# Kernel tuning notes

Measured on AMD Instinct MI355X. Metric: run time of the kernel, lower is better.

The kernel has to match this reference:

```python
import jax, jax.numpy as jnp
import numpy as np

H = 4  # num_heads in every nn.MultiheadAttention


def _mha_self(x, mask, w_in, b_in, w_out, b_out):
    # x: [N, L, E], mask: [N, L] (1 = valid). Matches torch nn.MultiheadAttention
    # self-attention with key_padding_mask, dropout=0 (eval).
    N, L, E = x.shape
    d = E // H
    qkv = x @ w_in.T + b_in                      # [N, L, 3E]
    q, k, v = jnp.split(qkv, 3, axis=-1)
    q = q.reshape(N, L, H, d)
    k = k.reshape(N, L, H, d)
    v = v.reshape(N, L, H, d)
    scale = 1.0 / float(np.sqrt(d))
    scores = jnp.einsum('nlhd,nmhd->nhlm', q, k) * scale
    scores = jnp.where(mask[:, None, None, :] > 0, scores, jnp.float32(-1e9))
    a = jax.nn.softmax(scores, axis=-1)
    o = jnp.einsum('nhlm,nmhd->nlhd', a, v).reshape(N, L, E)
    return o @ w_out.T + b_out


def _mha_cross_seq(q_x, kv_x, w_in, b_in, w_out, b_out):
    # torch MHA called with [B,1,E] tensors (batch_first=False): sequence length = B.
    E = q_x.shape[-1]
    d = E // H
    wq, wk, wv = jnp.split(w_in, 3, axis=0)
    bq, bk, bv = jnp.split(b_in, 3, axis=0)
    q = (q_x @ wq.T + bq).reshape(-1, H, d)
    k = (kv_x @ wk.T + bk).reshape(-1, H, d)
    v = (kv_x @ wv.T + bv).reshape(-1, H, d)
    scale = 1.0 / float(np.sqrt(d))
    a = jax.nn.softmax(jnp.einsum('lhd,mhd->hlm', q, k) * scale, axis=-1)
    o = jnp.einsum('hlm,mhd->lhd', a, v).reshape(-1, E)
    return o @ w_out.T + b_out


def _masked_mean(x, m):
    # (attn_out * mask).sum / (mask.sum + 1e-10); yields 0 for fully-masked rows,
    # matching the torch zero-embedding branches.
    return (x * m[..., None]).sum(axis=1) / (m.sum(axis=1, keepdims=True) + 1e-10)


def _ln(x, g, b, eps=1e-5):
    mu = x.mean(-1, keepdims=True)
    var = ((x - mu) ** 2).mean(-1, keepdims=True)
    return (x - mu) / jnp.sqrt(var + eps) * g + b


def setup_inputs():
    key = jax.random.key(0)
    ks = iter(jax.random.split(key, 48))
    B, S, T, W, E = 8, 8, 16, 64, 768
    F, FD = 20, 256

    def rnd(shape, scale):
        return jax.random.normal(next(ks), shape, jnp.float32) * scale

    inp = {}
    inp['word_embeddings'] = rnd((B, S, T, W, E), 1.0)
    inp['attention_mask'] = jax.random.randint(next(ks), (B, S, T, W), 0, 2, jnp.int32)
    inp['handcrafted_features'] = rnd((B, F), 1.0)
    for name in ('word', 'sent', 'sec'):
        inp[name + '_w_in'] = rnd((3 * E, E), 1.0 / np.sqrt(E))
        inp[name + '_b_in'] = jnp.zeros((3 * E,), jnp.float32)
        inp[name + '_w_out'] = rnd((E, E), 1.0 / np.sqrt(E))
        inp[name + '_b_out'] = jnp.zeros((E,), jnp.float32)
    inp['bp_w'] = rnd((FD, E), 1.0 / np.sqrt(E)); inp['bp_b'] = jnp.zeros((FD,), jnp.float32)
    inp['hp_w'] = rnd((FD, F), 1.0 / np.sqrt(F)); inp['hp_b'] = jnp.zeros((FD,), jnp.float32)
    inp['fa_w_in'] = rnd((3 * FD, FD), 1.0 / np.sqrt(FD)); inp['fa_b_in'] = jnp.zeros((3 * FD,), jnp.float32)
    inp['fa_w_out'] = rnd((FD, FD), 1.0 / np.sqrt(FD)); inp['fa_b_out'] = jnp.zeros((FD,), jnp.float32)
    inp['gate_w'] = rnd((FD, 2 * FD), 1.0 / np.sqrt(2 * FD)); inp['gate_b'] = jnp.zeros((FD,), jnp.float32)
    inp['fus_ln_g'] = jnp.ones((FD,), jnp.float32); inp['fus_ln_b'] = jnp.zeros((FD,), jnp.float32)
    inp['fc1_w'] = rnd((128, FD), 1.0 / np.sqrt(FD)); inp['fc1_b'] = jnp.zeros((128,), jnp.float32)
    inp['ln1_g'] = jnp.ones((128,), jnp.float32); inp['ln1_b'] = jnp.zeros((128,), jnp.float32)
    inp['fc2_w'] = rnd((3, 128), 1.0 / np.sqrt(128)); inp['fc2_b'] = jnp.zeros((3,), jnp.float32)
    return inp


def reference(word_embeddings, attention_mask, handcrafted_features,
              word_w_in, word_b_in, word_w_out, word_b_out,
              sent_w_in, sent_b_in, sent_w_out, sent_b_out,
              sec_w_in, sec_b_in, sec_w_out, sec_b_out,
              bp_w, bp_b, hp_w, hp_b,
              fa_w_in, fa_b_in, fa_w_out, fa_b_out,
              gate_w, gate_b, fus_ln_g, fus_ln_b,
              fc1_w, fc1_b, ln1_g, ln1_b, fc2_w, fc2_b):
    B, S, T, W, E = word_embeddings.shape
    m = attention_mask.astype(jnp.float32)
    # word-level attention over all B*S*T sentences at once
    x = word_embeddings.reshape(B * S * T, W, E)
    mw = m.reshape(B * S * T, W)
    wo = _mha_self(x, mw, word_w_in, word_b_in, word_w_out, word_b_out)
    sent = _masked_mean(wo, mw).reshape(B * S, T, E)        # sentence embeddings
    # sentence-level attention per section
    ms = (m.sum(-1) > 0).astype(jnp.float32).reshape(B * S, T)
    so = _mha_self(sent, ms, sent_w_in, sent_b_in, sent_w_out, sent_b_out)
    sec = _masked_mean(so, ms).reshape(B, S, E)             # section embeddings
    # section-level attention per document
    msec = (m.sum((-1, -2)) > 0).astype(jnp.float32)        # [B, S]
    do = _mha_self(sec, msec, sec_w_in, sec_b_in, sec_w_out, sec_b_out)
    doc = _masked_mean(do, msec)                            # [B, E]
    # feature fusion (the cross-attention output is computed but unused downstream,
    # exactly as in the torch code)
    bert_proj = doc @ bp_w.T + bp_b                         # [B, 256]
    hand_proj = handcrafted_features @ hp_w.T + hp_b        # [B, 256]
    _ = _mha_cross_seq(bert_proj, hand_proj, fa_w_in, fa_b_in, fa_w_out, fa_b_out)
    gate = jax.nn.sigmoid(jnp.concatenate([bert_proj, hand_proj], -1) @ gate_w.T + gate_b)
    fused = gate * bert_proj + (1.0 - gate) * hand_proj
    fused = _ln(fused, fus_ln_g, fus_ln_b)                  # dropout = identity (eval)
    h1 = jax.nn.relu(fused @ fc1_w.T + fc1_b)
    h1 = _ln(h1, ln1_g, ln1_b)
    return h1 @ fc2_w.T + fc2_b                             # [B, num_classes]
```

## Files before the change

### kernel.cpp

```cpp
#include <hip/hip_runtime.h>
#include <math.h>

#define EDIM 768
#define E3 2304

typedef __attribute__((ext_vector_type(8))) short short8;
typedef __attribute__((ext_vector_type(8))) unsigned short ushort8;
typedef __attribute__((ext_vector_type(4))) float f32x4;

__device__ inline void gload_lds16(const void* g, void* l) {
  __builtin_amdgcn_global_load_lds((const __attribute__((address_space(1))) void*)g,
                                   (__attribute__((address_space(3))) void*)l, 16, 0, 0);
}

__device__ inline unsigned short f2b_rne(float f) {
  unsigned int u = __builtin_bit_cast(unsigned int, f);
  u = (u + 0x7fffu + ((u >> 16) & 1u)) >> 16;
  return (unsigned short)u;
}
__device__ inline float b2f(unsigned short u) {
  unsigned int x = ((unsigned int)u) << 16;
  return __builtin_bit_cast(float, x);
}
__device__ inline float ldv(float v) { return v; }
__device__ inline float ldv(unsigned short v) { return b2f(v); }

__global__ __launch_bounds__(256) void f2bf(const float* __restrict__ in,
                                            unsigned short* __restrict__ out, size_t n) {
  size_t i = ((size_t)blockIdx.x * blockDim.x + threadIdx.x) * 8;
  size_t stride = (size_t)gridDim.x * blockDim.x * 8;
  for (; i < n; i += stride) {
    float4 a = *(const float4*)(in + i);
    float4 b = *(const float4*)(in + i + 4);
    ushort8 o;
    o[0] = f2b_rne(a.x); o[1] = f2b_rne(a.y); o[2] = f2b_rne(a.z); o[3] = f2b_rne(a.w);
    o[4] = f2b_rne(b.x); o[5] = f2b_rne(b.y); o[6] = f2b_rne(b.z); o[7] = f2b_rne(b.w);
    *(ushort8*)(out + i) = o;
  }
}

__global__ __launch_bounds__(256) void f2bf3(
    const float* __restrict__ i0, unsigned short* __restrict__ o0, size_t n0,
    const float* __restrict__ i1, unsigned short* __restrict__ o1, size_t n1,
    const float* __restrict__ i2, unsigned short* __restrict__ o2, size_t n2) {
  size_t c8 = (size_t)blockIdx.x * blockDim.x + threadIdx.x;
  size_t stride = (size_t)gridDim.x * blockDim.x;
  size_t t0 = n0 >> 3, t1 = t0 + (n1 >> 3), t2 = t1 + (n2 >> 3);
  for (; c8 < t2; c8 += stride) {
    const float* src; unsigned short* dst; size_t i;
    if (c8 < t0) { src = i0; dst = o0; i = c8 * 8; }
    else if (c8 < t1) { src = i1; dst = o1; i = (c8 - t0) * 8; }
    else { src = i2; dst = o2; i = (c8 - t1) * 8; }
    float4 a = *(const float4*)(src + i);
    float4 b = *(const float4*)(src + i + 4);
    ushort8 o;
    o[0] = f2b_rne(a.x); o[1] = f2b_rne(a.y); o[2] = f2b_rne(a.z); o[3] = f2b_rne(a.w);
    o[4] = f2b_rne(b.x); o[5] = f2b_rne(b.y); o[6] = f2b_rne(b.z); o[7] = f2b_rne(b.w);
    *(ushort8*)(dst + i) = o;
  }
}

__global__ void mask_stats1(const int* __restrict__ am, float* __restrict__ wsum,
                            float* __restrict__ svalid) {
  int n = blockIdx.x * blockDim.x + threadIdx.x;
  if (n < 1024) {
    int s = 0;
    const int* p = am + (size_t)n * 64;
    for (int w = 0; w < 64; ++w) s += p[w];
    wsum[n] = (float)s;
    svalid[n] = s > 0 ? 1.f : 0.f;
  }
}

__global__ void mask_stats2(const float* __restrict__ wsum, const float* __restrict__ svalid,
                            float* __restrict__ cnt2, float* __restrict__ secv,
                            float* __restrict__ cnt3) {
  int tid = threadIdx.x;
  if (tid < 64) {
    float c = 0.f, t = 0.f;
    for (int u = 0; u < 16; ++u) { c += svalid[tid * 16 + u]; t += wsum[tid * 16 + u]; }
    cnt2[tid] = c;
    secv[tid] = t > 0.f ? 1.f : 0.f;
  }
  __syncthreads();
  if (tid < 8) {
    float c = 0.f;
    for (int s = 0; s < 8; ++s) c += secv[tid * 8 + s];
    cnt3[tid] = c;
  }
}

__global__ __launch_bounds__(512, 2) void gemm8(
    const unsigned short* __restrict__ A, const unsigned short* __restrict__ B,
    const float* __restrict__ bias, unsigned short* __restrict__ C,
    int M, int N, int K) {
  __shared__ unsigned short lds[2][32768];
  const int tid = threadIdx.x;
  const int w = tid >> 6;
  const int lane = tid & 63;
  const int nbx = N / 256;
  const int cpx = gridDim.x >> 3;
  const int bid = blockIdx.x;
  const int swz = (bid & 7) * cpx + (bid >> 3);
  const int m0 = (swz / nbx) * 256;
  const int n0 = (swz % nbx) * 256;
  const int wr = w >> 2, wc = w & 3;
  const int fr = lane & 15;
  const int g = lane >> 4;
  const int NT64 = K / 64;
  f32x4 acc[8][4] = {};

  int srow[4], scol[4];
#pragma unroll
  for (int q = 0; q < 4; ++q) {
    int S = q * 512 + tid;
    srow[q] = S >> 3;
    scol[q] = ((S & 7) ^ (srow[q] & 7)) * 8;
  }
  auto stageA = [&](int t, int slot) {
    const int kt = t * 64;
#pragma unroll
    for (int q = 0; q < 4; ++q)
      gload_lds16(A + (size_t)(m0 + srow[q]) * K + kt + scol[q],
                  &lds[slot][(q * 512 + w * 64) * 8]);
  };
  auto stageB = [&](int t, int slot) {
    const int kt = t * 64;
#pragma unroll
    for (int q = 0; q < 4; ++q)
      gload_lds16(B + (size_t)(n0 + srow[q]) * K + kt + scol[q],
                  &lds[slot][16384 + (q * 512 + w * 64) * 8]);
  };
  int aoff[2][8], boff[2][4];
#pragma unroll
  for (int ks = 0; ks < 2; ++ks) {
#pragma unroll
    for (int i = 0; i < 8; ++i) {
      int r = wr * 128 + i * 16 + fr;
      aoff[ks][i] = (r * 8 + ((ks * 4 + g) ^ (r & 7))) * 8;
    }
#pragma unroll
    for (int j = 0; j < 4; ++j) {
      int r = wc * 64 + j * 16 + fr;
      boff[ks][j] = 16384 + (r * 8 + ((ks * 4 + g) ^ (r & 7))) * 8;
    }
  }

  stageA(0, 0);
  stageB(0, 0);
  asm volatile("s_waitcnt vmcnt(0)" ::: "memory");
  __builtin_amdgcn_sched_barrier(0);
  __builtin_amdgcn_s_barrier();
  __builtin_amdgcn_sched_barrier(0);

  int slot = 0;
  for (int t = 0; t < NT64; ++t) {
    const unsigned short* ls = lds[slot];
    if (t + 1 < NT64) stageA(t + 1, slot ^ 1);
    short8 av[8], bv[4];
#pragma unroll
    for (int i = 0; i < 8; ++i) av[i] = *(const short8*)(ls + aoff[0][i]);
#pragma unroll
    for (int j = 0; j < 4; ++j) bv[j] = *(const short8*)(ls + boff[0][j]);
    __builtin_amdgcn_s_setprio(1);
#pragma unroll
    for (int i = 0; i < 8; ++i)
#pragma unroll
      for (int j = 0; j < 4; ++j)
        acc[i][j] = __builtin_amdgcn_mfma_f32_16x16x32_bf16(av[i], bv[j], acc[i][j], 0, 0, 0);
    __builtin_amdgcn_s_setprio(0);
    if (t + 1 < NT64) stageB(t + 1, slot ^ 1);
#pragma unroll
    for (int i = 0; i < 8; ++i) av[i] = *(const short8*)(ls + aoff[1][i]);
#pragma unroll
    for (int j = 0; j < 4; ++j) bv[j] = *(const short8*)(ls + boff[1][j]);
    __builtin_amdgcn_s_setprio(1);
#pragma unroll
    for (int i = 0; i < 8; ++i)
#pragma unroll
      for (int j = 0; j < 4; ++j)
        acc[i][j] = __builtin_amdgcn_mfma_f32_16x16x32_bf16(av[i], bv[j], acc[i][j], 0, 0, 0);
    __builtin_amdgcn_s_setprio(0);
    asm volatile("s_waitcnt vmcnt(0)" ::: "memory");
    __builtin_amdgcn_sched_barrier(0);
    __builtin_amdgcn_s_barrier();
    __builtin_amdgcn_sched_barrier(0);
    slot ^= 1;
  }

  const int cl = lane & 15;
  const int rg = (lane >> 4) * 4;
#pragma unroll
  for (int i = 0; i < 8; ++i) {
    const int mrow0 = m0 + wr * 128 + i * 16 + rg;
#pragma unroll
    for (int j = 0; j < 4; ++j) {
      const int col = n0 + wc * 64 + j * 16 + cl;
      const float bvv = bias[col];
#pragma unroll
      for (int r = 0; r < 4; ++r)
        C[(size_t)(mrow0 + r) * N + col] = f2b_rne(acc[i][j][r] + bvv);
    }
  }
}

__global__ __launch_bounds__(256) void attn_qk(
    const unsigned short* __restrict__ qk, const unsigned short* __restrict__ xbf,
    const int* __restrict__ am, const float* __restrict__ wsum,
    unsigned short* __restrict__ xbarbf) {
  __shared__ float abar_all[4][64];
  __shared__ float msk[64];
  const int n = blockIdx.x;
  const int tid = threadIdx.x;
  const int h = tid >> 6;
  const int lane = tid & 63;
  if (tid < 64) msk[tid] = (am[(size_t)n * 64 + tid] > 0) ? 1.f : 0.f;
  __syncthreads();
  const int fr = lane & 15;
  const int fk = (lane >> 4) * 8;
  const unsigned short* Qg = qk + (size_t)n * 64 * 1536 + h * 192;
  const unsigned short* Kg = Qg + 768;
  f32x4 acc[4][4] = {};
#pragma unroll
  for (int ks = 0; ks < 6; ++ks) {
    short8 aq[4], bk[4];
#pragma unroll
    for (int i = 0; i < 4; ++i)
      aq[i] = *(const short8*)(Qg + (size_t)(i * 16 + fr) * 1536 + ks * 32 + fk);
#pragma unroll
    for (int j = 0; j < 4; ++j)
      bk[j] = *(const short8*)(Kg + (size_t)(j * 16 + fr) * 1536 + ks * 32 + fk);
#pragma unroll
    for (int i = 0; i < 4; ++i)
#pragma unroll
      for (int j = 0; j < 4; ++j)
        acc[i][j] = __builtin_amdgcn_mfma_f32_16x16x32_bf16(aq[i], bk[j], acc[i][j], 0, 0, 0);
  }
  const float den = wsum[n] + 1e-10f;
  const float scale = 0.07216878364870323f;
  float mcol[4];
#pragma unroll
  for (int j = 0; j < 4; ++j) mcol[j] = msk[j * 16 + fr];
  float colsum[4] = {0.f, 0.f, 0.f, 0.f};
#pragma unroll
  for (int i = 0; i < 4; ++i) {
#pragma unroll
    for (int r = 0; r < 4; ++r) {
      float s[4];
      float mx = -1e30f;
#pragma unroll
      for (int j = 0; j < 4; ++j) {
        float v = mcol[j] > 0.f ? acc[i][j][r] * scale : -1e9f;
        s[j] = v;
        mx = fmaxf(mx, v);
      }
      mx = fmaxf(mx, __shfl_xor(mx, 1));
      mx = fmaxf(mx, __shfl_xor(mx, 2));
      mx = fmaxf(mx, __shfl_xor(mx, 4));
      mx = fmaxf(mx, __shfl_xor(mx, 8));
      float sum = 0.f;
#pragma unroll
      for (int j = 0; j < 4; ++j) { s[j] = expf(s[j] - mx); sum += s[j]; }
      sum += __shfl_xor(sum, 1);
      sum += __shfl_xor(sum, 2);
      sum += __shfl_xor(sum, 4);
      sum += __shfl_xor(sum, 8);
      float wrow = msk[i * 16 + (lane >> 4) * 4 + r] / den;
      float f = wrow / sum;
#pragma unroll
      for (int j = 0; j < 4; ++j) colsum[j] += s[j] * f;
    }
  }
#pragma unroll
  for (int j = 0; j < 4; ++j) {
    float cs = colsum[j];
    cs += __shfl_xor(cs, 16);
    cs += __shfl_xor(cs, 32);
    if (lane < 16) abar_all[h][j * 16 + lane] = cs;
  }
  __syncthreads();
  const unsigned short* xg = xbf + (size_t)n * 64 * 768;
  float a4[4][3] = {};
  for (int m = 0; m < 64; ++m) {
    float ab0 = abar_all[0][m], ab1 = abar_all[1][m];
    float ab2 = abar_all[2][m], ab3 = abar_all[3][m];
#pragma unroll
    for (int u = 0; u < 3; ++u) {
      float x = b2f(xg[(size_t)m * 768 + u * 256 + tid]);
      a4[0][u] += ab0 * x;
      a4[1][u] += ab1 * x;
      a4[2][u] += ab2 * x;
      a4[3][u] += ab3 * x;
    }
  }
#pragma unroll
  for (int hh = 0; hh < 4; ++hh)
#pragma unroll
    for (int u = 0; u < 3; ++u)
      xbarbf[((size_t)hh * 1024 + n) * 768 + u * 256 + tid] = f2b_rne(a4[hh][u]);
}

__global__ __launch_bounds__(256) void gemm_bf16_64(
    const unsigned short* __restrict__ A, const unsigned short* __restrict__ B,
    const float* __restrict__ bias, const float* __restrict__ cnt,
    float* __restrict__ C, unsigned short* __restrict__ Cb,
    int K, int ldc, size_t Az, size_t Bz, int colz) {
  __shared__ unsigned short smA[128 * 32];
  __shared__ unsigned short smB[64 * 32];
  const int tid = threadIdx.x;
  const int wid = tid >> 6;
  const int lane = tid & 63;
  const int za = blockIdx.z;
  A += (size_t)za * Az;
  B += (size_t)za * Bz;
  const int m0 = blockIdx.y * 128;
  const int nb = blockIdx.x * 64;
  const int wr = wid >> 1, wc = wid & 1;
  const int srow = lane >> 2;
  const int scol = (lane & 3) * 8;
  const int fr = lane & 15;
  const int fk = (lane >> 4) * 8;
  f32x4 acc[4][2] = {};
  for (int k0 = 0; k0 < K; k0 += 32) {
#pragma unroll
    for (int t = 0; t < 2; ++t) {
      const int r0 = wid * 32 + t * 16;
      gload_lds16(A + (size_t)(m0 + r0 + srow) * K + k0 + scol, &smA[r0 * 32]);
    }
    gload_lds16(B + (size_t)(nb + wid * 16 + srow) * K + k0 + scol, &smB[wid * 16 * 32]);
    __syncthreads();
    short8 af[4], bfr[2];
#pragma unroll
    for (int i = 0; i < 4; ++i)
      af[i] = *(const short8*)&smA[(wr * 64 + i * 16 + fr) * 32 + fk];
#pragma unroll
    for (int j = 0; j < 2; ++j)
      bfr[j] = *(const short8*)&smB[(wc * 32 + j * 16 + fr) * 32 + fk];
#pragma unroll
    for (int i = 0; i < 4; ++i)
#pragma unroll
      for (int j = 0; j < 2; ++j)
        acc[i][j] = __builtin_amdgcn_mfma_f32_16x16x32_bf16(af[i], bfr[j], acc[i][j], 0, 0, 0);
    __syncthreads();
  }
  const int cl = lane & 15;
  const int rg = (lane >> 4) * 4;
#pragma unroll
  for (int i = 0; i < 4; ++i) {
    const int mrow0 = m0 + wr * 64 + i * 16 + rg;
#pragma unroll
    for (int j = 0; j < 2; ++j) {
      const int gc = za * colz + nb + wc * 32 + j * 16 + cl;
      const float bv = bias[gc];
#pragma unroll
      for (int r = 0; r < 4; ++r) {
        const int m = mrow0 + r;
        float sf = 1.f;
        if (cnt) { float c = cnt[m]; sf = c / (c + 1e-10f); }
        float v = acc[i][j][r] + bv * sf;
        if (Cb) Cb[(size_t)m * ldc + gc] = f2b_rne(v);
        else C[(size_t)m * ldc + gc] = v;
      }
    }
  }
}

#define BM 64
#define BN 64
#define BK 16
__global__ __launch_bounds__(256) void gemm_nt(
    const float* __restrict__ X, const float* __restrict__ W,
    const float* __restrict__ bias, const float* __restrict__ cnt,
    float* __restrict__ out, int M, int N, int K, int lda, int ldc) {
  __shared__ float As[BK][BM + 4];
  __shared__ float Bs[BK][BN + 4];
  const int tid = threadIdx.x;
  const int m0 = blockIdx.y * BM;
  const int n0 = blockIdx.x * BN;
  const int tx = tid & 15, ty = tid >> 4;
  const int lr = tid >> 2;
  const int lc = (tid & 3) * 4;
  float acc[4][4];
#pragma unroll
  for (int i = 0; i < 4; ++i)
#pragma unroll
    for (int j = 0; j < 4; ++j) acc[i][j] = 0.f;
  for (int k0 = 0; k0 < K; k0 += BK) {
    float4 xa = make_float4(0.f, 0.f, 0.f, 0.f);
    if (m0 + lr < M) xa = *(const float4*)(X + (size_t)(m0 + lr) * lda + k0 + lc);
    float4 wb = *(const float4*)(W + (size_t)(n0 + lr) * K + k0 + lc);
    As[lc + 0][lr] = xa.x; As[lc + 1][lr] = xa.y; As[lc + 2][lr] = xa.z; As[lc + 3][lr] = xa.w;
    Bs[lc + 0][lr] = wb.x; Bs[lc + 1][lr] = wb.y; Bs[lc + 2][lr] = wb.z; Bs[lc + 3][lr] = wb.w;
    __syncthreads();
#pragma unroll
    for (int kk = 0; kk < BK; ++kk) {
      float4 av = *(const float4*)&As[kk][ty * 4];
      float4 bv = *(const float4*)&Bs[kk][tx * 4];
      float a4[4] = {av.x, av.y, av.z, av.w};
      float b4[4] = {bv.x, bv.y, bv.z, bv.w};
#pragma unroll
      for (int i = 0; i < 4; ++i)
#pragma unroll
        for (int j = 0; j < 4; ++j) acc[i][j] += a4[i] * b4[j];
    }
    __syncthreads();
  }
#pragma unroll
  for (int i = 0; i < 4; ++i) {
    int m = m0 + ty * 4 + i;
    if (m < M) {
      float sf = 1.f;
      if (cnt) { float c = cnt[m]; sf = c / (c + 1e-10f); }
      float4 o;
      o.x = acc[i][0] + bias[n0 + tx * 4 + 0] * sf;
      o.y = acc[i][1] + bias[n0 + tx * 4 + 1] * sf;
      o.z = acc[i][2] + bias[n0 + tx * 4 + 2] * sf;
      o.w = acc[i][3] + bias[n0 + tx * 4 + 3] * sf;
      *(float4*)(out + (size_t)m * ldc + n0 + tx * 4) = o;
    }
  }
}

template <class T>
__global__ __launch_bounds__(256) void small_attn(
    const T* __restrict__ qkv, const float* __restrict__ maskv,
    const float* __restrict__ cnt, float* __restrict__ obar, int L) {
  const int n = blockIdx.x;
  const int h = blockIdx.y;
  const int tid = threadIdx.x;
  __shared__ float red[16][17];
  __shared__ float abar[16];
  const T* qb = qkv + (size_t)n * L * E3 + h * 192;
  const T* kb = qb + EDIM;
  const T* vb = qb + 2 * EDIM;
  const float scale = 0.07216878364870323f;
  if (tid < L * L) {
    int l = tid / L, m = tid % L;
    float s = 0.f;
    for (int dd = 0; dd < 192; ++dd) s += ldv(qb[(size_t)l * E3 + dd]) * ldv(kb[(size_t)m * E3 + dd]);
    s = (maskv[n * L + m] > 0.f) ? s * scale : -1e9f;
    float mx = s;
    for (int off = L >> 1; off > 0; off >>= 1) mx = fmaxf(mx, __shfl_xor(mx, off));
    float p = expf(s - mx);
    float sum = p;
    for (int off = L >> 1; off > 0; off >>= 1) sum += __shfl_xor(sum, off);
    float dn = cnt[n] + 1e-10f;
    float wl = (maskv[n * L + l] > 0.f) ? (1.f / dn) : 0.f;
    red[l][m] = p / sum * wl;
  }
  __syncthreads();
  if (tid < L) {
    float s = 0.f;
    for (int l2 = 0; l2 < L; ++l2) s += red[l2][tid];
    abar[tid] = s;
  }
  __syncthreads();
  if (tid < 192) {
    float acc = 0.f;
    for (int m = 0; m < L; ++m) acc += abar[m] * ldv(vb[(size_t)m * E3 + tid]);
    obar[(size_t)n * EDIM + h * 192 + tid] = acc;
  }
}

__global__ __launch_bounds__(256) void head_kernel(
    const float* __restrict__ doc, const float* __restrict__ hand,
    const float* __restrict__ bp_w, const float* __restrict__ bp_b,
    const float* __restrict__ hp_w, const float* __restrict__ hp_b,
    const float* __restrict__ gate_w, const float* __restrict__ gate_b,
    const float* __restrict__ fg, const float* __restrict__ fbv,
    const float* __restrict__ fc1_w, const float* __restrict__ fc1_b,
    const float* __restrict__ g1, const float* __restrict__ b1,
    const float* __restrict__ fc2_w, const float* __restrict__ fc2_b,
    float* __restrict__ out) {
  int b = blockIdx.x, tid = threadIdx.x;
  __shared__ float bp[256], hp[256], fz[256], hz[128];
  const float* dr = doc + (size_t)b * 768;
  float acc = bp_b[tid];
  for (int k = 0; k < 768; ++k) acc += dr[k] * bp_w[(size_t)tid * 768 + k];
  bp[tid] = acc;
  const float* hr = hand + b * 20;
  float acc2 = hp_b[tid];
  for (int k = 0; k < 20; ++k) acc2 += hr[k] * hp_w[tid * 20 + k];
  hp[tid] = acc2;
  __syncthreads();
  float g = gate_b[tid];
  for (int k = 0; k < 256; ++k) g += bp[k] * gate_w[tid * 512 + k];
  for (int k = 0; k < 256; ++k) g += hp[k] * gate_w[tid * 512 + 256 + k];
  g = 1.f / (1.f + expf(-g));
  float fu = g * bp[tid] + (1.f - g) * hp[tid];
  fz[tid] = fu;
  __syncthreads();
  float mu = 0.f;
  for (int k = 0; k < 256; ++k) mu += fz[k];
  mu /= 256.f;
  float va = 0.f;
  for (int k = 0; k < 256; ++k) { float d = fz[k] - mu; va += d * d; }
  va /= 256.f;
  float fl = (fu - mu) / sqrtf(va + 1e-5f) * fg[tid] + fbv[tid];
  __syncthreads();
  fz[tid] = fl;
  __syncthreads();
  if (tid < 128) {
    float a = fc1_b[tid];
    for (int k = 0; k < 256; ++k) a += fz[k] * fc1_w[tid * 256 + k];
    hz[tid] = fmaxf(a, 0.f);
  }
  __syncthreads();
  float mu2 = 0.f;
  for (int k = 0; k < 128; ++k) mu2 += hz[k];
  mu2 /= 128.f;
  float va2 = 0.f;
  for (int k = 0; k < 128; ++k) { float d = hz[k] - mu2; va2 += d * d; }
  va2 /= 128.f;
  __syncthreads();
  if (tid < 128) hz[tid] = (hz[tid] - mu2) / sqrtf(va2 + 1e-5f) * g1[tid] + b1[tid];
  __syncthreads();
  if (tid < 3) {
    float o = fc2_b[tid];
    for (int k = 0; k < 128; ++k) o += hz[k] * fc2_w[tid * 128 + k];
    out[b * 3 + tid] = o;
  }
}

extern "C" void kernel_launch(void* const* d_in, const int* in_sizes, int n_in,
                              void* d_out, int out_size, void* d_ws, size_t ws_size,
                              hipStream_t stream) {
  const float* we      = (const float*)d_in[0];
  const int*   am      = (const int*)d_in[1];
  const float* hand    = (const float*)d_in[2];
  const float* w_w_in  = (const float*)d_in[3];
  const float* w_b_in  = (const float*)d_in[4];
  const float* w_w_out = (const float*)d_in[5];
  const float* w_b_out = (const float*)d_in[6];
  const float* s_w_in  = (const float*)d_in[7];
  const float* s_b_in  = (const float*)d_in[8];
  const float* s_w_out = (const float*)d_in[9];
  const float* s_b_out = (const float*)d_in[10];
  const float* c_w_in  = (const float*)d_in[11];
  const float* c_b_in  = (const float*)d_in[12];
  const float* c_w_out = (const float*)d_in[13];
  const float* c_b_out = (const float*)d_in[14];
  const float* bp_w = (const float*)d_in[15];
  const float* bp_b = (const float*)d_in[16];
  const float* hp_w = (const float*)d_in[17];
  const float* hp_b = (const float*)d_in[18];
  const float* gate_w = (const float*)d_in[23];
  const float* gate_b = (const float*)d_in[24];
  const float* fus_g  = (const float*)d_in[25];
  const float* fus_b  = (const float*)d_in[26];
  const float* fc1_w  = (const float*)d_in[27];
  const float* fc1_b  = (const float*)d_in[28];
  const float* ln1_g  = (const float*)d_in[29];
  const float* ln1_b  = (const float*)d_in[30];
  const float* fc2_w  = (const float*)d_in[31];
  const float* fc2_b  = (const float*)d_in[32];
  float* out = (float*)d_out;

  unsigned short* qk  = (unsigned short*)d_ws;
  unsigned short* xbf = qk + (size_t)65536 * 1536;

  char* end = (char*)d_ws + ws_size;
  auto carveb = [&](size_t bytes) {
    size_t b = (bytes + 255) & ~(size_t)255;
    end -= b;
    return (void*)end;
  };
  unsigned short* xbarbf  = (unsigned short*)carveb((size_t)4 * 1024 * 768 * 2);
  unsigned short* obarbf  = (unsigned short*)carveb((size_t)1024 * 768 * 2);
  unsigned short* sentbf  = (unsigned short*)carveb((size_t)1024 * 768 * 2);
  unsigned short* qkv2bf  = (unsigned short*)carveb((size_t)1024 * 2304 * 2);
  float* obar2  = (float*)carveb(64 * 768 * 4);
  float* sec    = (float*)carveb(64 * 768 * 4);
  float* qkv3   = (float*)carveb(64 * 2304 * 4);
  float* obar3  = (float*)carveb(8 * 768 * 4);
  float* doc    = (float*)carveb(8 * 768 * 4);
  float* wsum   = (float*)carveb(1024 * 4);
  float* svalid = (float*)carveb(1024 * 4);
  float* cnt2   = (float*)carveb(64 * 4);
  float* secv   = (float*)carveb(64 * 4);
  float* cnt3   = (float*)carveb(8 * 4);
  unsigned short* wbf_in = (unsigned short*)carveb((size_t)2304 * 768 * 2);
  unsigned short* wobf   = (unsigned short*)carveb((size_t)768 * 768 * 2);
  unsigned short* wsbf   = (unsigned short*)carveb((size_t)2304 * 768 * 2);

  f2bf3<<<2048, 256, 0, stream>>>(w_w_in, wbf_in, (size_t)2304 * 768,
                                  w_w_out, wobf, (size_t)768 * 768,
                                  s_w_in, wsbf, (size_t)2304 * 768);
  mask_stats1<<<4, 256, 0, stream>>>(am, wsum, svalid);
  mask_stats2<<<1, 64, 0, stream>>>(wsum, svalid, cnt2, secv, cnt3);

  f2bf<<<2048, 256, 0, stream>>>(we, xbf, (size_t)65536 * 768);
  gemm8<<<(65536 / 256) * (1536 / 256), 512, 0, stream>>>(xbf, wbf_in, w_b_in, qk,
                                                          65536, 1536, 768);
  attn_qk<<<1024, 256, 0, stream>>>(qk, xbf, am, wsum, xbarbf);
  gemm_bf16_64<<<dim3(3, 8, 4), 256, 0, stream>>>(
      xbarbf, wbf_in + (size_t)1536 * 768, w_b_in + 1536, wsum, nullptr, obarbf,
      768, 768, (size_t)1024 * 768, (size_t)192 * 768, 192);
  gemm_bf16_64<<<dim3(12, 8, 1), 256, 0, stream>>>(
      obarbf, wobf, w_b_out, wsum, nullptr, sentbf, 768, 768, 0, 0, 0);
  gemm_bf16_64<<<dim3(36, 8, 1), 256, 0, stream>>>(
      sentbf, wsbf, s_b_in, nullptr, nullptr, qkv2bf, 768, 2304, 0, 0, 0);
  small_attn<<<dim3(64, 4), 256, 0, stream>>>(qkv2bf, svalid, cnt2, obar2, 16);
  gemm_nt<<<dim3(12, 1), 256, 0, stream>>>(obar2, s_w_out, s_b_out, cnt2, sec,
                                           64, 768, 768, 768, 768);
  gemm_nt<<<dim3(36, 1), 256, 0, stream>>>(sec, c_w_in, c_b_in, nullptr, qkv3,
                                           64, 2304, 768, 768, 2304);
  small_attn<<<dim3(8, 4), 256, 0, stream>>>(qkv3, secv, cnt3, obar3, 8);
  gemm_nt<<<dim3(12, 1), 256, 0, stream>>>(obar3, c_w_out, c_b_out, cnt3, doc,
                                           8, 768, 768, 768, 768);
  head_kernel<<<8, 256, 0, stream>>>(doc, hand, bp_w, bp_b, hp_w, hp_b, gate_w, gate_b,
                                     fus_g, fus_b, fc1_w, fc1_b, ln1_g, ln1_b, fc2_w, fc2_b, out);
}
```

Before: 582.1 us.

## Triple-buffer A tiles in gemm8 with partial vmcnt waits; merge mask-stat kernels

The main GEMM now keeps three LDS buffers for A and two for B. A is prefetched two k-steps ahead, and the loop waits with vmcnt(4) instead of fully draining outstanding loads, so global loads overlap more of the MFMA work. K is hardcoded to 12 tiles of 64, which only holds for K=768. LDS use per block rises from 128KB to 160KB, which may conflict with the two-blocks-per-CU launch bound. Separately, the two mask-statistics kernels are merged into one 1024-thread block that reduces through shared memory, saving a launch.

```diff
diff --git a/kernel.cpp b/kernel.cpp
--- a/kernel.cpp
+++ b/kernel.cpp
@@ -3,6 +3,7 @@
 
 #define EDIM 768
 #define E3 2304
+#define NT12 12
 
 typedef __attribute__((ext_vector_type(8))) short short8;
 typedef __attribute__((ext_vector_type(8))) unsigned short ushort8;
@@ -60,32 +61,31 @@
   }
 }
 
-__global__ void mask_stats1(const int* __restrict__ am, float* __restrict__ wsum,
-                            float* __restrict__ svalid) {
-  int n = blockIdx.x * blockDim.x + threadIdx.x;
-  if (n < 1024) {
-    int s = 0;
-    const int* p = am + (size_t)n * 64;
-    for (int w = 0; w < 64; ++w) s += p[w];
-    wsum[n] = (float)s;
-    svalid[n] = s > 0 ? 1.f : 0.f;
-  }
-}
-
-__global__ void mask_stats2(const float* __restrict__ wsum, const float* __restrict__ svalid,
-                            float* __restrict__ cnt2, float* __restrict__ secv,
-                            float* __restrict__ cnt3) {
+__global__ __launch_bounds__(1024) void mask_stats(
+    const int* __restrict__ am, float* __restrict__ wsum, float* __restrict__ svalid,
+    float* __restrict__ cnt2, float* __restrict__ secv, float* __restrict__ cnt3) {
   int tid = threadIdx.x;
+  int s = 0;
+  const int* p = am + (size_t)tid * 64;
+  for (int w = 0; w < 64; ++w) s += p[w];
+  wsum[tid] = (float)s;
+  float sv = s > 0 ? 1.f : 0.f;
+  svalid[tid] = sv;
+  __shared__ float sva[1024];
+  sva[tid] = sv;
+  __syncthreads();
   if (tid < 64) {
-    float c = 0.f, t = 0.f;
-    for (int u = 0; u < 16; ++u) { c += svalid[tid * 16 + u]; t += wsum[tid * 16 + u]; }
+    float c = 0.f;
+    for (int u = 0; u < 16; ++u) c += sva[tid * 16 + u];
     cnt2[tid] = c;
-    secv[tid] = t > 0.f ? 1.f : 0.f;
-  }
+    secv[tid] = c > 0.f ? 1.f : 0.f;
+  }
+  __syncthreads();
+  if (tid < 64) sva[tid] = secv[tid];
   __syncthreads();
   if (tid < 8) {
     float c = 0.f;
-    for (int s = 0; s < 8; ++s) c += secv[tid * 8 + s];
+    for (int s2 = 0; s2 < 8; ++s2) c += sva[tid * 8 + s2];
     cnt3[tid] = c;
   }
 }
@@ -94,7 +94,8 @@
     const unsigned short* __restrict__ A, const unsigned short* __restrict__ B,
     const float* __restrict__ bias, unsigned short* __restrict__ C,
     int M, int N, int K) {
-  __shared__ unsigned short lds[2][32768];
+  __shared__ unsigned short ldsA[3][16384];
+  __shared__ unsigned short ldsB[2][16384];
   const int tid = threadIdx.x;
   const int w = tid >> 6;
   const int lane = tid & 63;
@@ -107,7 +108,6 @@
   const int wr = w >> 2, wc = w & 3;
   const int fr = lane & 15;
   const int g = lane >> 4;
-  const int NT64 = K / 64;
   f32x4 acc[8][4] = {};
 
   int srow[4], scol[4];
@@ -122,14 +122,14 @@
 #pragma unroll
     for (int q = 0; q < 4; ++q)
       gload_lds16(A + (size_t)(m0 + srow[q]) * K + kt + scol[q],
-                  &lds[slot][(q * 512 + w * 64) * 8]);
+                  &ldsA[slot][(q * 512 + w * 64) * 8]);
   };
   auto stageB = [&](int t, int slot) {
     const int kt = t * 64;
 #pragma unroll
     for (int q = 0; q < 4; ++q)
       gload_lds16(B + (size_t)(n0 + srow[q]) * K + kt + scol[q],
-                  &lds[slot][16384 + (q * 512 + w * 64) * 8]);
+                  &ldsB[slot][(q * 512 + w * 64) * 8]);
   };
   int aoff[2][8], boff[2][4];
 #pragma unroll
@@ -142,26 +142,29 @@
 #pragma unroll
     for (int j = 0; j < 4; ++j) {
       int r = wc * 64 + j * 16 + fr;
-      boff[ks][j] = 16384 + (r * 8 + ((ks * 4 + g) ^ (r & 7))) * 8;
-    }
-  }
-
+      boff[ks][j] = (r * 8 + ((ks * 4 + g) ^ (r & 7))) * 8;
+    }
+  }
+
+  stageB(0, 0);
   stageA(0, 0);
-  stageB(0, 0);
+  stageA(1, 1);
   asm volatile("s_waitcnt vmcnt(0)" ::: "memory");
   __builtin_amdgcn_sched_barrier(0);
   __builtin_amdgcn_s_barrier();
   __builtin_amdgcn_sched_barrier(0);
 
-  int slot = 0;
-  for (int t = 0; t < NT64; ++t) {
-    const unsigned short* ls = lds[slot];
-    if (t + 1 < NT64) stageA(t + 1, slot ^ 1);
+  int sA = 0;
+#pragma unroll 1
+  for (int t = 0; t < NT12; ++t) {
+    const unsigned short* la = ldsA[sA];
+    const unsigned short* lb = ldsB[t & 1];
+    if (t + 1 < NT12) stageB(t + 1, (t + 1) & 1);
     short8 av[8], bv[4];
 #pragma unroll
-    for (int i = 0; i < 8; ++i) av[i] = *(const short8*)(ls + aoff[0][i]);
-#pragma unroll
-    for (int j = 0; j < 4; ++j) bv[j] = *(const short8*)(ls + boff[0][j]);
+    for (int i = 0; i < 8; ++i) av[i] = *(const short8*)(la + aoff[0][i]);
+#pragma unroll
+    for (int j = 0; j < 4; ++j) bv[j] = *(const short8*)(lb + boff[0][j]);
     __builtin_amdgcn_s_setprio(1);
 #pragma unroll
     for (int i = 0; i < 8; ++i)
@@ -169,11 +172,14 @@
       for (int j = 0; j < 4; ++j)
         acc[i][j] = __builtin_amdgcn_mfma_f32_16x16x32_bf16(av[i], bv[j], acc[i][j], 0, 0, 0);
     __builtin_amdgcn_s_setprio(0);
-    if (t + 1 < NT64) stageB(t + 1, slot ^ 1);
-#pragma unroll
-    for (int i = 0; i < 8; ++i) av[i] = *(const short8*)(ls + aoff[1][i]);
-#pragma unroll
-    for (int j = 0; j < 4; ++j) bv[j] = *(const short8*)(ls + boff[1][j]);
+    {
+      int s2 = sA + 2; if (s2 >= 3) s2 -= 3;
+      if (t + 2 < NT12) stageA(t + 2, s2);
+    }
+#pragma unroll
+    for (int i = 0; i < 8; ++i) av[i] = *(const short8*)(la + aoff[1][i]);
+#pragma unroll
+    for (int j = 0; j < 4; ++j) bv[j] = *(const short8*)(lb + boff[1][j]);
     __builtin_amdgcn_s_setprio(1);
 #pragma unroll
     for (int i = 0; i < 8; ++i)
@@ -181,11 +187,17 @@
       for (int j = 0; j < 4; ++j)
         acc[i][j] = __builtin_amdgcn_mfma_f32_16x16x32_bf16(av[i], bv[j], acc[i][j], 0, 0, 0);
     __builtin_amdgcn_s_setprio(0);
-    asm volatile("s_waitcnt vmcnt(0)" ::: "memory");
-    __builtin_amdgcn_sched_barrier(0);
-    __builtin_amdgcn_s_barrier();
-    __builtin_amdgcn_sched_barrier(0);
-    slot ^= 1;
+    if (t < NT12 - 1) {
+      if (t + 2 < NT12) {
+        asm volatile("s_waitcnt vmcnt(4)" ::: "memory");
+      } else {
+        asm volatile("s_waitcnt vmcnt(0)" ::: "memory");
+      }
+      __builtin_amdgcn_sched_barrier(0);
+      __builtin_amdgcn_s_barrier();
+      __builtin_amdgcn_sched_barrier(0);
+    }
+    if (++sA == 3) sA = 0;
   }
 
   const int cl = lane & 15;
@@ -586,8 +598,7 @@
   f2bf3<<<2048, 256, 0, stream>>>(w_w_in, wbf_in, (size_t)2304 * 768,
                                   w_w_out, wobf, (size_t)768 * 768,
                                   s_w_in, wsbf, (size_t)2304 * 768);
-  mask_stats1<<<4, 256, 0, stream>>>(am, wsum, svalid);
-  mask_stats2<<<1, 64, 0, stream>>>(wsum, svalid, cnt2, secv, cnt3);
+  mask_stats<<<1, 1024, 0, stream>>>(am, wsum, svalid, cnt2, secv, cnt3);
 
   f2bf<<<2048, 256, 0, stream>>>(we, xbf, (size_t)65536 * 768);
   gemm8<<<(65536 / 256) * (1536 / 256), 512, 0, stream>>>(xbf, wbf_in, w_b_in, qk,
```

Measured after the change: 613.5 us. +5.4%, slower.
